# Kernel tuning notes

Hardware: AMD Instinct MI355X
Metric: run time of the kernel (lower is better)

## Reference

```python
import jax, jax.numpy as jnp
import numpy as np

BUCKET = 32   # bucket_size hard-coded in module
HEADS = 8
LN_EPS = 1e-5
SELF_ATTN_VALUE = -5e4  # TOKEN_SELF_ATTN_VALUE from reformer-pytorch


def _layer_norm(x, g, b):
    m = jnp.mean(x, axis=-1, keepdims=True)
    v = jnp.mean((x - m) ** 2, axis=-1, keepdims=True)
    return (x - m) / jnp.sqrt(v + LN_EPS) * g + b


def _lsh_attention(qk, v, rot):
    # qk, v: (B=b*h, T, Dh); rot: (Dh, n_buckets//2); n_hashes = 1
    B, T, D = qk.shape
    n_buckets = T // BUCKET
    # hash: random rotations, argmax over [r, -r]
    r = jnp.einsum('btf,fi->bti', qk, rot)                 # (B, T, n_buckets//2)
    r = jnp.concatenate([r, -r], axis=-1)                  # (B, T, n_buckets)
    buckets = jnp.argmax(r, axis=-1)                       # (B, T) int
    t = jnp.arange(T)
    key = buckets * T + t                                  # unique sort key
    sticker = jnp.argsort(key, axis=-1)                    # (B, T) permutation
    undo = jnp.argsort(sticker, axis=-1)
    sqk = jnp.take_along_axis(qk, sticker[..., None], axis=1)
    sv = jnp.take_along_axis(v, sticker[..., None], axis=1)
    # chunk into n_buckets chunks of size BUCKET
    bq_t = sticker.reshape(B, n_buckets, BUCKET)
    bq = sqk.reshape(B, n_buckets, BUCKET, D)
    bv = sv.reshape(B, n_buckets, BUCKET, D)
    nrm = jnp.sqrt(jnp.sum(bq * bq, axis=-1, keepdims=True))
    bk = bq / jnp.maximum(nrm, 1e-12)                      # shared-QK: keys are unit-norm queries
    def look_one_back(xx):
        return jnp.concatenate([xx, jnp.roll(xx, 1, axis=1)], axis=2)
    bk = look_one_back(bk)
    bvv = look_one_back(bv)
    bkv_t = look_one_back(bq_t)
    dots = jnp.einsum('bcie,bcje->bcij', bq, bk) * (D ** -0.5)  # (B, C, 32, 64)
    self_mask = bq_t[:, :, :, None] == bkv_t[:, :, None, :]
    dots = jnp.where(self_mask, SELF_ATTN_VALUE, dots)
    attn = jax.nn.softmax(dots, axis=-1)
    bo = jnp.einsum('bcij,bcje->bcie', attn, bvv)
    so = bo.reshape(B, T, D)
    return jnp.take_along_axis(so, undo[..., None], axis=1)   # unsort (n_hashes=1 -> probs=1)


def _lsh_self_attention(h, w_qk, w_v, w_out, b_out, rot):
    b, t, d = h.shape
    dh = d // HEADS
    qk = (h @ w_qk).reshape(b, t, HEADS, dh).transpose(0, 2, 1, 3).reshape(b * HEADS, t, dh)
    vv = (h @ w_v).reshape(b, t, HEADS, dh).transpose(0, 2, 1, 3).reshape(b * HEADS, t, dh)
    o = _lsh_attention(qk, vv, rot)
    o = o.reshape(b, HEADS, t, dh).transpose(0, 2, 1, 3).reshape(b, t, d)
    return o @ w_out + b_out


def setup_inputs() -> dict:
    key = jax.random.key(0)
    ks = jax.random.split(key, 8)
    B, T, D, F = 8, 4096, 512, 2048
    dh, nb = D // HEADS, T // BUCKET
    s = 0.02
    return {
        'x': jax.random.normal(ks[0], (B, T, D), jnp.float32),
        'w_qk': jax.random.normal(ks[1], (D, D), jnp.float32) * s,
        'w_v': jax.random.normal(ks[2], (D, D), jnp.float32) * s,
        'w_out': jax.random.normal(ks[3], (D, D), jnp.float32) * s,
        'b_out': jnp.zeros((D,), jnp.float32),
        'ln1_g': jnp.ones((D,), jnp.float32),
        'ln1_b': jnp.zeros((D,), jnp.float32),
        'w_ff1': jax.random.normal(ks[4], (D, F), jnp.float32) * s,
        'b_ff1': jnp.zeros((F,), jnp.float32),
        'w_ff2': jax.random.normal(ks[5], (F, D), jnp.float32) * s,
        'b_ff2': jnp.zeros((D,), jnp.float32),
        'ln2_g': jnp.ones((D,), jnp.float32),
        'ln2_b': jnp.zeros((D,), jnp.float32),
        'rotations': jax.random.normal(ks[6], (dh, nb // 2), jnp.float32),
    }


def reference(x, w_qk, w_v, w_out, b_out, ln1_g, ln1_b, w_ff1, b_ff1,
              w_ff2, b_ff2, ln2_g, ln2_b, rotations):
    # y1 = x + Attn(LN1(x)); y2 = x + FFN(LN2(y1)); out = mean(y1, y2)
    h1 = _layer_norm(x, ln1_g, ln1_b)
    y1 = x + _lsh_self_attention(h1, w_qk, w_v, w_out, b_out, rotations)
    h2 = _layer_norm(y1, ln2_g, ln2_b)
    ffn = jax.nn.relu(h2 @ w_ff1 + b_ff1) @ w_ff2 + b_ff2
    y2 = x + ffn
    return 0.5 * (y1 + y2)
```

## Files before the change

kernel.cpp:

```cpp
#include <hip/hip_runtime.h>
#include <stdint.h>

typedef _Float16 f16;
typedef _Float16 f16x8 __attribute__((ext_vector_type(8)));
typedef float    f32x4 __attribute__((ext_vector_type(4)));
typedef unsigned long long u64;

__device__ __forceinline__ void gload16(const void* g, void* l) {
  __builtin_amdgcn_global_load_lds(
      (__attribute__((address_space(1))) void*)g,
      (__attribute__((address_space(3))) void*)l, 16, 0, 0);
}

#define MFMA_QUAD(q, af) \
  _Pragma("unroll") for (int m2 = 0; m2 < 2; ++m2) \
  _Pragma("unroll") for (int nt = 0; nt < 4; ++nt) \
  _Pragma("unroll") for (int kk = 0; kk < 2; ++kk) \
    acc[(q)*2 + m2][nt] = __builtin_amdgcn_mfma_f32_16x16x32_f16( \
        af[m2][kk], bf[nt][kk], acc[(q)*2 + m2][nt], 0, 0, 0);

#define RD_A(dst, abase, q2) \
  _Pragma("unroll") for (int m2 = 0; m2 < 2; ++m2) \
  _Pragma("unroll") for (int kk = 0; kk < 2; ++kk) { \
    const int lr = (q2)*32 + m2*16 + l15; \
    dst[m2][kk] = *(const f16x8*)&abase[lr*64 + (((kk*4 + l4) ^ (lr & 7)) << 3)]; }

#define RD_B(bbase) \
  _Pragma("unroll") for (int nt = 0; nt < 4; ++nt) \
  _Pragma("unroll") for (int kk = 0; kk < 2; ++kk) { \
    const int lr = brow + nt*16 + l15; \
    bf[nt][kk] = *(const f16x8*)&bbase[lr*64 + (((kk*4 + l4) ^ (lr & 7)) << 3)]; }

#define PH_PRE() \
  __builtin_amdgcn_s_barrier(); \
  asm volatile("s_waitcnt lgkmcnt(0)" ::: "memory"); \
  __builtin_amdgcn_sched_barrier(0); \
  __builtin_amdgcn_s_setprio(1);

#define PH_POST() \
  __builtin_amdgcn_s_setprio(0); \
  __builtin_amdgcn_s_barrier(); \
  __builtin_amdgcn_sched_barrier(0);

template<int EPI>
__global__ __launch_bounds__(512, 2)
void gemm256(const f16* __restrict__ A, int lda,
             const f16* __restrict__ Bt, int ldb,
             int K, int N,
             float* __restrict__ outf, f16* __restrict__ outh,
             f16* __restrict__ outh2,
             const float* __restrict__ bias,
             const f16* __restrict__ sxyh,
             const float* __restrict__ add1)
{
  __shared__ __align__(16) f16 lds[65536];
  const int tid = threadIdx.x, lane = tid & 63;
  const int wid = tid >> 6;
  const int wm = wid >> 2, wn = wid & 3;
  const int l15 = lane & 15, l4 = lane >> 4;

  const int gx = gridDim.x;
  int lid = blockIdx.y * gx + blockIdx.x;
  const int cpx = (gx * gridDim.y) >> 3;
  lid = (lid & 7) * cpx + (lid >> 3);
  const long bm0 = (long)(lid / gx) * 256;
  const long bn0 = (long)(lid % gx) * 256;

  const int rs = tid >> 3, cs = tid & 7;
  const int cg = cs ^ (rs & 7);
  const int nkt = K >> 6;
  const int nmask = nkt - 1;

  auto stageA = [&](int d, int half, int kt) {
    f16* dst = &lds[(d * 4 + half) * 8192];
    const long kb = (long)kt * 64 + cg * 8;
    const f16* src = A + (bm0 + half * 128) * lda + kb;
#pragma unroll
    for (int rr = 0; rr < 2; ++rr) {
      const int row = rs + rr * 64;
      gload16(src + (long)row * lda, dst + row * 64 + cs * 8);
    }
  };
  auto stageB = [&](int d, int half, int kt) {
    f16* dst = &lds[(d * 4 + 2 + half) * 8192];
    const long kb = (long)kt * 64 + cg * 8;
    const f16* src = Bt + (bn0 + half * 128) * ldb + kb;
#pragma unroll
    for (int rr = 0; rr < 2; ++rr) {
      const int row = rs + rr * 64;
      gload16(src + (long)row * ldb, dst + row * 64 + cs * 8);
    }
  };

  const f16* aBase0 = &lds[(0 + wm) * 8192];
  const f16* aBase1 = &lds[(4 + wm) * 8192];
  const f16* bBase0 = &lds[(2 + (wn >> 1)) * 8192];
  const f16* bBase1 = &lds[(6 + (wn >> 1)) * 8192];
  const int brow = (wn & 1) * 64;

  f32x4 acc[8][4];
#pragma unroll
  for (int i = 0; i < 8; ++i)
#pragma unroll
    for (int j = 0; j < 4; ++j) acc[i][j] = f32x4{0.f, 0.f, 0.f, 0.f};
  f16x8 bf[4][2], afA[2][2], afB[2][2];

  stageB(0, 0, 0); stageB(0, 1, 0); stageA(0, 0, 0); stageA(0, 1, 0);
  asm volatile("s_waitcnt vmcnt(4)" ::: "memory");
  stageB(1, 0, 1); stageB(1, 1, 1); stageA(1, 0, 1);
  asm volatile("s_waitcnt vmcnt(6)" ::: "memory");
  __builtin_amdgcn_s_barrier();
  __builtin_amdgcn_sched_barrier(0);

  for (int j = 0; j < nkt; j += 2) {
    const int t2 = (j + 2) & nmask, t3 = (j + 3) & nmask;
    RD_B(bBase0); RD_A(afA, aBase0, 0);
    stageA(1, 1, j + 1);
    asm volatile("s_waitcnt lgkmcnt(8)" ::: "memory");
    PH_PRE(); MFMA_QUAD(0, afA); PH_POST();
    RD_A(afB, aBase0, 1); RD_A(afA, aBase0, 2);
    stageB(0, 0, t2);
    PH_PRE(); MFMA_QUAD(1, afB); PH_POST();
    RD_A(afB, aBase0, 3);
    stageB(0, 1, t2);
    PH_PRE(); MFMA_QUAD(2, afA); PH_POST();
    stageA(0, 0, t2);
    asm volatile("s_waitcnt vmcnt(6)" ::: "memory");
    PH_PRE(); MFMA_QUAD(3, afB); PH_POST();
    RD_B(bBase1); RD_A(afA, aBase1, 0);
    stageA(0, 1, t2);
    asm volatile("s_waitcnt lgkmcnt(8)" ::: "memory");
    PH_PRE(); MFMA_QUAD(0, afA); PH_POST();
    RD_A(afB, aBase1, 1); RD_A(afA, aBase1, 2);
    stageB(1, 0, t3);
    PH_PRE(); MFMA_QUAD(1, afB); PH_POST();
    RD_A(afB, aBase1, 3);
    stageB(1, 1, t3);
    PH_PRE(); MFMA_QUAD(2, afA); PH_POST();
    stageA(1, 0, t3);
    asm volatile("s_waitcnt vmcnt(6)" ::: "memory");
    PH_PRE(); MFMA_QUAD(3, afB); PH_POST();
  }
  asm volatile("s_waitcnt vmcnt(0)" ::: "memory");

  if constexpr (EPI == 17) {
    const int hcol = (int)(bn0 >> 6) + wn;
    const int is_v = hcol >> 3, h = hcol & 7;
    f16* base = is_v ? outh2 : outh;
#pragma unroll
    for (int mt = 0; mt < 8; ++mt)
#pragma unroll
      for (int r = 0; r < 4; ++r) {
        const long grow = bm0 + wm * 128 + mt * 16 + l4 * 4 + r;
        const int bb = (int)(grow >> 12), tt = (int)(grow & 4095);
        f16* dst = base + (((long)bb * 8 + h) * 4096 + tt) * 64;
#pragma unroll
        for (int nt = 0; nt < 4; ++nt)
          dst[nt * 16 + l15] = (f16)acc[mt][nt][0 * 4 + 0];
      }
  }
#pragma unroll
  for (int mt = 0; mt < 8; ++mt)
#pragma unroll
    for (int nt = 0; nt < 4; ++nt)
#pragma unroll
      for (int r = 0; r < 4; ++r) {
        const long grow = bm0 + wm * 128 + mt * 16 + l4 * 4 + r;
        const long gcol = bn0 + wn * 64 + nt * 16 + l15;
        const float c = acc[mt][nt][r];
        if constexpr (EPI == 12) {
          const long idx = grow * (long)N + gcol;
          outf[idx] = c + bias[gcol] + add1[idx];
        } else if constexpr (EPI == 13) {
          const long idx = grow * (long)N + gcol;
          outh[idx] = (f16)fmaxf(c + bias[gcol], 0.f);
        } else if constexpr (EPI == 40) {
          const long idx = grow * (long)N + gcol;
          outf[idx] = (float)sxyh[idx] + 0.5f * c;
        } else if constexpr (EPI == 41) {
          const long idx = grow * (long)N + gcol;
          outf[idx] += 0.5f * (c + bias[gcol]);
        } else if constexpr (EPI == 17) {
          const int bb = (int)(grow >> 12), tt = (int)(grow & 4095);
          const int hcol = (int)(bn0 >> 6) + wn;
          const int is_v = hcol >> 3, h = hcol & 7;
          f16* base = is_v ? outh2 : outh;
          base[(((long)bb * 8 + h) * 4096 + tt) * 64 + nt * 16 + l15] = (f16)c;
        }
      }
}

__global__ __launch_bounds__(256)
void ln_kernel(const float* __restrict__ in, const float* __restrict__ gam,
               const float* __restrict__ bet, f16* __restrict__ out,
               int ldo, int split, const float* __restrict__ xin,
               f16* __restrict__ sxy)
{
  const long row = (long)blockIdx.x * 4 + (threadIdx.x >> 6);
  const int lane = threadIdx.x & 63;
  const float4* p = (const float4*)(in + row * 512);
  const float4 a = p[lane * 2], b = p[lane * 2 + 1];
  float xv[8] = {a.x, a.y, a.z, a.w, b.x, b.y, b.z, b.w};
  float s = 0.f;
#pragma unroll
  for (int i = 0; i < 8; ++i) s += xv[i];
#pragma unroll
  for (int m = 32; m; m >>= 1) s += __shfl_xor(s, m);
  const float mean = s * (1.f / 512.f);
  float vs = 0.f;
#pragma unroll
  for (int i = 0; i < 8; ++i) { const float d = xv[i] - mean; vs += d * d; }
#pragma unroll
  for (int m = 32; m; m >>= 1) vs += __shfl_xor(vs, m);
  const float rstd = 1.f / sqrtf(vs * (1.f / 512.f) + 1e-5f);
  const float4* gp = (const float4*)gam;
  const float4* bp = (const float4*)bet;
  const float4 g0 = gp[lane * 2], g1 = gp[lane * 2 + 1];
  const float4 b0 = bp[lane * 2], b1 = bp[lane * 2 + 1];
  const float gg[8] = {g0.x, g0.y, g0.z, g0.w, g1.x, g1.y, g1.z, g1.w};
  const float bb[8] = {b0.x, b0.y, b0.z, b0.w, b1.x, b1.y, b1.z, b1.w};
  f16x8 vh, vl;
#pragma unroll
  for (int i = 0; i < 8; ++i) {
    const float y = (xv[i] - mean) * rstd * gg[i] + bb[i];
    const f16 hi = (f16)y;
    vh[i] = hi;
    vl[i] = (f16)((y - (float)hi) * 64.f);
  }
  f16* o = out + row * ldo + lane * 8;
  *(f16x8*)o = vh;
  if (split) *(f16x8*)(o + 512) = vl;
  if (sxy) {
    const float4* xp = (const float4*)(xin + row * 512);
    const float4 x0 = xp[lane * 2], x1 = xp[lane * 2 + 1];
    const float xx[8] = {x0.x, x0.y, x0.z, x0.w, x1.x, x1.y, x1.z, x1.w};
    f16x8 vsx;
#pragma unroll
    for (int i = 0; i < 8; ++i) vsx[i] = (f16)(0.5f * (xv[i] + xx[i]));
    *(f16x8*)(sxy + row * 512 + lane * 8) = vsx;
  }
}

__global__ __launch_bounds__(256)
void transpose_f16(const float* __restrict__ src, f16* __restrict__ dst, int K, int N)
{
  __shared__ float tile[32][33];
  const int tx = threadIdx.x & 31, ty = threadIdx.x >> 5;
  const long k0 = (long)blockIdx.y * 32, n0 = (long)blockIdx.x * 32;
#pragma unroll
  for (int i = 0; i < 4; ++i)
    tile[ty + i * 8][tx] = src[(k0 + ty + i * 8) * N + n0 + tx];
  __syncthreads();
#pragma unroll
  for (int i = 0; i < 4; ++i)
    dst[(n0 + ty + i * 8) * K + k0 + tx] = (f16)tile[tx][ty + i * 8];
}

__global__ __launch_bounds__(256)
void whash_f32(const float* __restrict__ wqk, const float* __restrict__ rot,
               float* __restrict__ WrT, f16* __restrict__ rotTh)
{
  if (blockIdx.x == 0 && blockIdx.y == 0) {
    for (int idx = threadIdx.x; idx < 4096; idx += 256) {
      const int d = idx >> 6, i = idx & 63;
      rotTh[i * 64 + d] = (f16)rot[idx];
    }
  }
  const int kk = blockIdx.x;
  const int n  = blockIdx.y * 256 + threadIdx.x;
  const int h = n >> 6, i = n & 63;
  float s = 0.f;
  for (int d = 0; d < 64; ++d)
    s += wqk[kk * 512 + h * 64 + d] * rot[d * 64 + i];
  WrT[(long)n * 512 + kk] = s;
}

__global__ __launch_bounds__(256)
void rhash4_kernel(const f16* __restrict__ gqk, const f16* __restrict__ rotTh,
                   int* __restrict__ buckets)
{
  const int tid = threadIdx.x, lane = tid & 63, w = tid >> 6;
  const int bh = blockIdx.x >> 5, tb = blockIdx.x & 31;
  const int t0 = tb * 128;
  const int l15 = lane & 15, l4 = lane >> 4;

  f16x8 br[2][4];
#pragma unroll
  for (int kk = 0; kk < 2; ++kk)
#pragma unroll
    for (int nt = 0; nt < 4; ++nt)
      br[kk][nt] = *(const f16x8*)&rotTh[(nt * 16 + l15) * 64 + kk * 32 + l4 * 8];

  const f16* gqb = gqk + ((long)bh * 4096 + t0) * 64;
  f16x8 aq[2][2];
#pragma unroll
  for (int kk = 0; kk < 2; ++kk)
#pragma unroll
    for (int mt = 0; mt < 2; ++mt)
      aq[kk][mt] = *(const f16x8*)&gqb[(long)(w * 32 + mt * 16 + l15) * 64 + kk * 32 + l4 * 8];

  f32x4 acc[2][4];
#pragma unroll
  for (int i = 0; i < 2; ++i)
#pragma unroll
    for (int j = 0; j < 4; ++j) acc[i][j] = f32x4{0.f, 0.f, 0.f, 0.f};
#pragma unroll
  for (int kk = 0; kk < 2; ++kk)
#pragma unroll
    for (int mt = 0; mt < 2; ++mt)
#pragma unroll
      for (int nt = 0; nt < 4; ++nt)
        acc[mt][nt] = __builtin_amdgcn_mfma_f32_16x16x32_f16(aq[kk][mt], br[kk][nt], acc[mt][nt], 0, 0, 0);

#pragma unroll
  for (int mt = 0; mt < 2; ++mt)
#pragma unroll
    for (int r = 0; r < 4; ++r) {
      const float v0 = acc[mt][0][r], v1 = acc[mt][1][r];
      const float v2 = acc[mt][2][r], v3 = acc[mt][3][r];
      unsigned int k0 = (__float_as_uint(fabsf(v0)) & ~63u) | (unsigned int)(63 - l15);
      unsigned int k1 = (__float_as_uint(fabsf(v1)) & ~63u) | (unsigned int)(47 - l15);
      unsigned int k2 = (__float_as_uint(fabsf(v2)) & ~63u) | (unsigned int)(31 - l15);
      unsigned int k3 = (__float_as_uint(fabsf(v3)) & ~63u) | (unsigned int)(15 - l15);
      float ss = v0 * v0 + v1 * v1 + v2 * v2 + v3 * v3;
#pragma unroll
      for (int m = 1; m < 16; m <<= 1) ss += __shfl_xor(ss, m);

      unsigned int mk = max(max(k0, k1), max(k2, k3));
#pragma unroll
      for (int m = 1; m < 16; m <<= 1) mk = max(mk, (unsigned int)__shfl_xor((int)mk, m));
      const unsigned int key1 = mk;
      const int col1 = 63 - (int)(key1 & 63u);
      const float m1f = __uint_as_float(key1 & ~63u);
      const int nt1 = col1 >> 4;
      const float vsel = (nt1 == 0) ? v0 : (nt1 == 1) ? v1 : (nt1 == 2) ? v2 : v3;
      const bool owner = (col1 & 15) == l15;
      const u64 bal = __ballot(owner && (vsel < 0.f));
      const int neg = (int)((bal >> (l4 * 16 + (col1 & 15))) & 1ull);
      const int bucket = col1 + (neg << 6);
      if (owner) {
        if (nt1 == 0) k0 = 0; else if (nt1 == 1) k1 = 0;
        else if (nt1 == 2) k2 = 0; else k3 = 0;
      }
      mk = max(max(k0, k1), max(k2, k3));
#pragma unroll
      for (int m = 1; m < 16; m <<= 1) mk = max(mk, (unsigned int)__shfl_xor((int)mk, m));
      const int col2 = 63 - (int)(mk & 63u);
      const float m2f = __uint_as_float(mk & ~63u);
      {
        const int nt2 = col2 >> 4;
        if ((col2 & 15) == l15) {
          if (nt2 == 0) k0 = 0; else if (nt2 == 1) k1 = 0;
          else if (nt2 == 2) k2 = 0; else k3 = 0;
        }
      }
      mk = max(max(k0, k1), max(k2, k3));
#pragma unroll
      for (int m = 1; m < 16; m <<= 1) mk = max(mk, (unsigned int)__shfl_xor((int)mk, m));
      const int col3 = 63 - (int)(mk & 63u);

      if (l15 == 0) {
        const int row = w * 32 + mt * 16 + l4 * 4 + r;
        const int bht = bh * 4096 + t0 + row;
        const float margin = m1f - m2f;
        const float rms = sqrtf(ss * (1.f / 64.f));
        const int flag = (margin < 0.015f * rms) ? 1 : 0;
        buckets[bht] = bucket | (col2 << 8) | (col3 << 16) | (flag << 24);
      }
    }
}

__global__ __launch_bounds__(256)
void fixup2_kernel(const f16* __restrict__ hsplit, const float* __restrict__ WrT,
                   int* __restrict__ buckets)
{
  const int wid = (blockIdx.x * 256 + threadIdx.x) >> 6;
  const int lane = threadIdx.x & 63;
  for (int batch = 0; batch < 4; ++batch) {
    const int base = wid * 256 + batch * 64;
    const int packed = buckets[base + lane];
    u64 bal = __ballot((packed >> 24) & 1);
    while (bal) {
      const int i = (int)__ffsll((long long)bal) - 1;
      bal &= bal - 1;
      const int row = base + i;
      const int pk = __shfl(packed, i);
      const int h = (row >> 12) & 7;
      const long hrow = (long)(row >> 15) * 4096 + (row & 4095);
      const f16* hp = hsplit + hrow * 1024 + lane * 8;
      const f16x8 hi = *(const f16x8*)hp;
      const f16x8 lo = *(const f16x8*)(hp + 512);
      float h1[8];
#pragma unroll
      for (int k = 0; k < 8; ++k) h1[k] = (float)hi[k] + (float)lo[k] * 0.015625f;
      const int cols[3] = { pk & 63, (pk >> 8) & 63, (pk >> 16) & 63 };
      float best = -1e30f; int bi = 999;
#pragma unroll
      for (int c = 0; c < 3; ++c) {
        const int cc = cols[c];
        const float* wp = WrT + ((long)(h * 64 + cc)) * 512 + lane * 8;
        const float4 w0 = *(const float4*)wp;
        const float4 w1 = *(const float4*)(wp + 4);
        float s = h1[0] * w0.x + h1[1] * w0.y + h1[2] * w0.z + h1[3] * w0.w
                + h1[4] * w1.x + h1[5] * w1.y + h1[6] * w1.z + h1[7] * w1.w;
#pragma unroll
        for (int m = 32; m; m >>= 1) s += __shfl_xor(s, m);
        if (s > best || (s == best && cc < bi)) { best = s; bi = cc; }
        const float ns = -s; const int ni = 64 + cc;
        if (ns > best || (ns == best && ni < bi)) { best = ns; bi = ni; }
      }
      if (lane == 0) buckets[row] = bi;
    }
  }
}

__global__ __launch_bounds__(256)
void sort_kernel(const int* __restrict__ buckets, int* __restrict__ sticker)
{
  __shared__ int bkt[4096];
  __shared__ unsigned int cnts[64][128];
  __shared__ unsigned char rnk[4096];
  __shared__ int tot[128];
  __shared__ int base[128];
  const int bh = blockIdx.x;
  const int tid = threadIdx.x;
  const int lane = tid & 63, wv = tid >> 6;

  for (int i = tid; i < 4096; i += 256) bkt[i] = buckets[(long)bh * 4096 + i] & 127;
  for (int i = tid; i < 64 * 128; i += 256) ((unsigned int*)cnts)[i] = 0u;
  __syncthreads();

  for (int it = 0; it < 16; ++it) {
    const int c = wv * 16 + it;
    const int t = c * 64 + lane;
    const int b = bkt[t];
    unsigned long long m = ~0ull;
#pragma unroll
    for (int k = 0; k < 7; ++k) {
      const bool bit = (b >> k) & 1;
      const unsigned long long bal = __ballot(bit);
      m &= bit ? bal : ~bal;
    }
    const int rk = (int)__popcll(m & ((1ull << lane) - 1ull));
    rnk[t] = (unsigned char)rk;
    if (rk == 0) cnts[c][b] = (unsigned int)__popcll(m);
  }
  __syncthreads();

  if (tid < 128) {
    unsigned int run = 0;
    for (int c = 0; c < 64; ++c) {
      const unsigned int x = cnts[c][tid];
      cnts[c][tid] = run;
      run += x;
    }
    tot[tid] = (int)run;
  }
  __syncthreads();
  if (tid == 0) {
    int run = 0;
    for (int b = 0; b < 128; ++b) { base[b] = run; run += tot[b]; }
  }
  __syncthreads();

  for (int it = 0; it < 16; ++it) {
    const int c = wv * 16 + it;
    const int t = c * 64 + lane;
    const int b = bkt[t];
    const int pos = base[b] + (int)cnts[c][b] + (int)rnk[t];
    sticker[(long)bh * 4096 + pos] = t;
  }
}

__global__ __launch_bounds__(256)
void attn2_kernel(const f16* __restrict__ gqk, const f16* __restrict__ gv,
                  const int* __restrict__ sticker, f16* __restrict__ o)
{
  __shared__ __align__(16) f16 sqk[160 * 64];
  __shared__ __align__(16) f16 sVT[64 * 168];
  __shared__ __align__(16) f16 sP[4][32 * 72];
  __shared__ float rnorm[160];
  __shared__ int st[160];

  const int tid = threadIdx.x, lane = tid & 63, w = tid >> 6;
  const int cg = blockIdx.x, bh = blockIdx.y;
  const int b = bh >> 3, h = bh & 7;
  const int p0 = cg * 128 - 32;
  const int l15 = lane & 15, l4 = lane >> 4;

  if (tid < 160) st[tid] = sticker[(long)bh * 4096 + ((p0 + tid) & 4095)] & 4095;
  __syncthreads();

  const f16* gqb = gqk + (long)bh * 4096 * 64;
#pragma unroll
  for (int it = 0; it < 5; ++it) {
    const int idx = it * 256 + tid;
    const int row = idx >> 3, ch = idx & 7;
    const int gsrc = ch ^ (row & 7);
    gload16(gqb + (long)st[row] * 64 + gsrc * 8, &sqk[idx * 8]);
  }

  const f16* gvb = gv + (long)bh * 4096 * 64;
  f16x8 va[5];
#pragma unroll
  for (int i = 0; i < 5; ++i) {
    const int row = w * 40 + i * 8 + (lane >> 3);
    va[i] = *(const f16x8*)&gvb[(long)st[row] * 64 + (lane & 7) * 8];
  }
#pragma unroll
  for (int i = 0; i < 5; ++i) {
    const int row = w * 40 + i * 8 + (lane >> 3);
    const int d0 = (lane & 7) * 8;
#pragma unroll
    for (int e = 0; e < 8; ++e) sVT[(d0 + e) * 168 + row] = va[i][e];
  }
  __syncthreads();

  if (tid < 160) {
    float s = 0.f;
#pragma unroll
    for (int g = 0; g < 8; ++g) {
      const f16x8 v = *(const f16x8*)&sqk[tid * 64 + ((g ^ (tid & 7)) << 3)];
#pragma unroll
      for (int e = 0; e < 8; ++e) { const float f = (float)v[e]; s += f * f; }
    }
    rnorm[tid] = 1.f / fmaxf(sqrtf(s), 1e-12f);
  }
  __syncthreads();

  f32x4 acc[2][4];
#pragma unroll
  for (int i = 0; i < 2; ++i)
#pragma unroll
    for (int j = 0; j < 4; ++j) acc[i][j] = f32x4{0.f, 0.f, 0.f, 0.f};

#pragma unroll
  for (int kk = 0; kk < 2; ++kk) {
    f16x8 aq[2], bk[4];
#pragma unroll
    for (int mt = 0; mt < 2; ++mt) {
      const int row = 32 + w * 32 + mt * 16 + l15;
      const int g = kk * 4 + l4;
      aq[mt] = *(const f16x8*)&sqk[row * 64 + ((g ^ (row & 7)) << 3)];
    }
#pragma unroll
    for (int nt = 0; nt < 4; ++nt) {
      const int row = w * 32 + nt * 16 + l15;
      const int g = kk * 4 + l4;
      bk[nt] = *(const f16x8*)&sqk[row * 64 + ((g ^ (row & 7)) << 3)];
    }
#pragma unroll
    for (int mt = 0; mt < 2; ++mt)
#pragma unroll
      for (int nt = 0; nt < 4; ++nt)
        acc[mt][nt] = __builtin_amdgcn_mfma_f32_16x16x32_f16(aq[mt], bk[nt], acc[mt][nt], 0, 0, 0);
  }

  float rn[4];
#pragma unroll
  for (int nt = 0; nt < 4; ++nt) rn[nt] = rnorm[w * 32 + nt * 16 + l15];

  float pinv[2][4];
#pragma unroll
  for (int mt = 0; mt < 2; ++mt)
#pragma unroll
    for (int r = 0; r < 4; ++r) {
      const int row_i = mt * 16 + l4 * 4 + r;
      float mx = -1e30f;
#pragma unroll
      for (int nt = 0; nt < 4; ++nt) {
        float v = acc[mt][nt][r] * 0.125f * rn[nt];
        if (nt * 16 + l15 == row_i + 32) v = -5e4f;
        acc[mt][nt][r] = v;
        mx = fmaxf(mx, v);
      }
#pragma unroll
      for (int m = 8; m; m >>= 1) mx = fmaxf(mx, __shfl_xor(mx, m));
      float ssum = 0.f;
#pragma unroll
      for (int nt = 0; nt < 4; ++nt) {
        const float pe = expf(acc[mt][nt][r] - mx);
        ssum += pe;
        sP[w][row_i * 72 + nt * 16 + l15] = (f16)pe;
      }
#pragma unroll
      for (int m = 8; m; m >>= 1) ssum += __shfl_xor(ssum, m);
      pinv[mt][r] = 1.f / ssum;
    }
  __syncthreads();

  f32x4 pacc[2][4];
#pragma unroll
  for (int i = 0; i < 2; ++i)
#pragma unroll
    for (int j = 0; j < 4; ++j) pacc[i][j] = f32x4{0.f, 0.f, 0.f, 0.f};

#pragma unroll
  for (int kk = 0; kk < 2; ++kk) {
    f16x8 ap[2], bv[4];
#pragma unroll
    for (int mt = 0; mt < 2; ++mt)
      ap[mt] = *(const f16x8*)&sP[w][(mt * 16 + l15) * 72 + kk * 32 + l4 * 8];
#pragma unroll
    for (int nt = 0; nt < 4; ++nt)
      bv[nt] = *(const f16x8*)&sVT[(nt * 16 + l15) * 168 + w * 32 + kk * 32 + l4 * 8];
#pragma unroll
    for (int mt = 0; mt < 2; ++mt)
#pragma unroll
      for (int nt = 0; nt < 4; ++nt)
        pacc[mt][nt] = __builtin_amdgcn_mfma_f32_16x16x32_f16(ap[mt], bv[nt], pacc[mt][nt], 0, 0, 0);
  }

  const long ob = (long)b * 4096 * 512 + h * 64;
#pragma unroll
  for (int mt = 0; mt < 2; ++mt)
#pragma unroll
    for (int r = 0; r < 4; ++r) {
      const int row_i = mt * 16 + l4 * 4 + r;
      const long t = st[32 + w * 32 + row_i];
      const float sc = pinv[mt][r];
#pragma unroll
      for (int nt = 0; nt < 4; ++nt)
        o[ob + t * 512 + nt * 16 + l15] = (f16)(pacc[mt][nt][r] * sc);
    }
}

extern "C" void kernel_launch(void* const* d_in, const int* in_sizes, int n_in,
                              void* d_out, int out_size, void* d_ws, size_t ws_size,
                              hipStream_t stream)
{
  const float* x     = (const float*)d_in[0];
  const float* w_qk  = (const float*)d_in[1];
  const float* w_v   = (const float*)d_in[2];
  const float* w_out = (const float*)d_in[3];
  const float* b_out = (const float*)d_in[4];
  const float* ln1g  = (const float*)d_in[5];
  const float* ln1b  = (const float*)d_in[6];
  const float* w_ff1 = (const float*)d_in[7];
  const float* b_ff1 = (const float*)d_in[8];
  const float* w_ff2 = (const float*)d_in[9];
  const float* b_ff2 = (const float*)d_in[10];
  const float* ln2g  = (const float*)d_in[11];
  const float* ln2b  = (const float*)d_in[12];
  const float* rot   = (const float*)d_in[13];
  float* out = (float*)d_out;

  char* ws = (char*)d_ws;
  f16* hsplit = (f16*)ws;
  f16* o_buf  = (f16*)ws;
  f16* sxy    = (f16*)ws;
  f16* h2     = (f16*)(ws + 33554432);
  f16* gqk    = (f16*)(ws + 67108864);
  f16* gv     = (f16*)(ws + 100663296);
  f16* abuf   = (f16*)(ws + 67108864);
  char* W0 = ws + 134217728;
  f16* wqkvT = (f16*)W0;
  f16* woutT = (f16*)(W0 + 1048576);
  f16* wff1T = (f16*)(W0 + 1572864);
  f16* wff2T = (f16*)(W0 + 3670016);
  float* WrT = (float*)(W0 + 5767168);
  int* buckets = (int*)(W0 + 6815744);
  int* sticker = (int*)(W0 + 7864320);
  f16* rotTh   = (f16*)(W0 + 8912896);

  const dim3 b256(256);
  const dim3 b512(512);
  transpose_f16<<<dim3(16, 16), b256, 0, stream>>>(w_qk,  wqkvT,             512, 512);
  transpose_f16<<<dim3(16, 16), b256, 0, stream>>>(w_v,   wqkvT + 512 * 512, 512, 512);
  transpose_f16<<<dim3(16, 16), b256, 0, stream>>>(w_out, woutT,             512, 512);
  transpose_f16<<<dim3(64, 16), b256, 0, stream>>>(w_ff1, wff1T,             512, 2048);
  transpose_f16<<<dim3(16, 64), b256, 0, stream>>>(w_ff2, wff2T,             2048, 512);
  whash_f32<<<dim3(512, 2), b256, 0, stream>>>(w_qk, rot, WrT, rotTh);
  ln_kernel<<<dim3(8192), b256, 0, stream>>>(x, ln1g, ln1b, hsplit, 1024, 1, nullptr, nullptr);
  gemm256<17><<<dim3(4, 128), b512, 0, stream>>>(hsplit, 1024, wqkvT, 512, 512, 1024,
      nullptr, gqk, gv, nullptr, nullptr, nullptr);
  rhash4_kernel<<<dim3(2048), b256, 0, stream>>>(gqk, rotTh, buckets);
  fixup2_kernel<<<dim3(256), b256, 0, stream>>>(hsplit, WrT, buckets);
  sort_kernel<<<dim3(64), b256, 0, stream>>>(buckets, sticker);
  attn2_kernel<<<dim3(32, 64), b256, 0, stream>>>(gqk, gv, sticker, o_buf);
  gemm256<12><<<dim3(2, 128), b512, 0, stream>>>(o_buf, 512, woutT, 512, 512, 512,
      out, nullptr, nullptr, b_out, nullptr, x);
  ln_kernel<<<dim3(8192), b256, 0, stream>>>(out, ln2g, ln2b, h2, 512, 0, x, sxy);
  for (int f = 0; f < 2; ++f) {
    gemm256<13><<<dim3(4, 128), b512, 0, stream>>>(h2, 512, wff1T + (long)f * 1024 * 512, 512,
        512, 1024, nullptr, abuf, nullptr, b_ff1 + f * 1024, nullptr, nullptr);
    if (f == 0)
      gemm256<40><<<dim3(2, 128), b512, 0, stream>>>(abuf, 1024, wff2T + 1024 * 0, 2048,
          1024, 512, out, nullptr, nullptr, b_ff2, sxy, nullptr);
    else
      gemm256<41><<<dim3(2, 128), b512, 0, stream>>>(abuf, 1024, wff2T + 1024, 2048,
          1024, 512, out, nullptr, nullptr, b_ff2, sxy, nullptr);
  }
}
```

Measured before the change: 491.3 us.

## Split FFN by rows instead of hidden dim; add dedicated 128-tile FFN2 GEMM

The feed-forward block was previously split along the hidden dimension (two 1024-wide halves), with the second FFN2 pass doing a read-modify-write on the output. It is now split into two row chunks, each computing the full 2048-wide FFN1 and then a new 128x128-tile GEMM kernel for FFN2 with K=2048 that writes the final output in one pass. The new FFN2 kernel uses a simple single-buffered LDS loop instead of the pipelined 256-tile kernel, which may reduce overlap but gives more blocks for the N=512 output. Dead epilogue variants and an unused pointer argument are removed, and a K-tile index is masked.

```diff
diff --git a/kernel.cpp b/kernel.cpp
--- a/kernel.cpp
+++ b/kernel.cpp
@@ -50,7 +50,6 @@
              float* __restrict__ outf, f16* __restrict__ outh,
              f16* __restrict__ outh2,
              const float* __restrict__ bias,
-             const f16* __restrict__ sxyh,
              const float* __restrict__ add1)
 {
   __shared__ __align__(16) f16 lds[65536];
@@ -115,7 +114,7 @@
   for (int j = 0; j < nkt; j += 2) {
     const int t2 = (j + 2) & nmask, t3 = (j + 3) & nmask;
     RD_B(bBase0); RD_A(afA, aBase0, 0);
-    stageA(1, 1, j + 1);
+    stageA(1, 1, (j + 1) & nmask);
     asm volatile("s_waitcnt lgkmcnt(8)" ::: "memory");
     PH_PRE(); MFMA_QUAD(0, afA); PH_POST();
     RD_A(afB, aBase0, 1); RD_A(afA, aBase0, 2);
@@ -143,22 +142,6 @@
   }
   asm volatile("s_waitcnt vmcnt(0)" ::: "memory");
 
-  if constexpr (EPI == 17) {
-    const int hcol = (int)(bn0 >> 6) + wn;
-    const int is_v = hcol >> 3, h = hcol & 7;
-    f16* base = is_v ? outh2 : outh;
-#pragma unroll
-    for (int mt = 0; mt < 8; ++mt)
-#pragma unroll
-      for (int r = 0; r < 4; ++r) {
-        const long grow = bm0 + wm * 128 + mt * 16 + l4 * 4 + r;
-        const int bb = (int)(grow >> 12), tt = (int)(grow & 4095);
-        f16* dst = base + (((long)bb * 8 + h) * 4096 + tt) * 64;
-#pragma unroll
-        for (int nt = 0; nt < 4; ++nt)
-          dst[nt * 16 + l15] = (f16)acc[mt][nt][0 * 4 + 0];
-      }
-  }
 #pragma unroll
   for (int mt = 0; mt < 8; ++mt)
 #pragma unroll
@@ -174,12 +157,6 @@
         } else if constexpr (EPI == 13) {
           const long idx = grow * (long)N + gcol;
           outh[idx] = (f16)fmaxf(c + bias[gcol], 0.f);
-        } else if constexpr (EPI == 40) {
-          const long idx = grow * (long)N + gcol;
-          outf[idx] = (float)sxyh[idx] + 0.5f * c;
-        } else if constexpr (EPI == 41) {
-          const long idx = grow * (long)N + gcol;
-          outf[idx] += 0.5f * (c + bias[gcol]);
         } else if constexpr (EPI == 17) {
           const int bb = (int)(grow >> 12), tt = (int)(grow & 4095);
           const int hcol = (int)(bn0 >> 6) + wn;
@@ -187,6 +164,88 @@
           f16* base = is_v ? outh2 : outh;
           base[(((long)bb * 8 + h) * 4096 + tt) * 64 + nt * 16 + l15] = (f16)c;
         }
+      }
+}
+
+__global__ __launch_bounds__(512)
+void gemm8_ffn2(const f16* __restrict__ A,
+                const f16* __restrict__ Bt,
+                const f16* __restrict__ sxyh,
+                const float* __restrict__ bias,
+                float* __restrict__ outf)
+{
+  __shared__ __align__(16) f16 sA[128 * 64];
+  __shared__ __align__(16) f16 sB[128 * 64];
+  const int tid  = threadIdx.x;
+  const int lane = tid & 63;
+  const int wv   = tid >> 6;
+  const int wm   = wv >> 2, wn = wv & 3;
+  const int l15  = lane & 15, l4 = lane >> 4;
+
+  const int gx = gridDim.x;
+  int lid = blockIdx.y * gx + blockIdx.x;
+  const int cpx = (gx * gridDim.y) >> 3;
+  lid = (lid & 7) * cpx + (lid >> 3);
+  const long bm0 = (long)(lid / gx) * 128;
+  const long bn0 = (long)(lid % gx) * 128;
+
+  f32x4 acc[4][2];
+#pragma unroll
+  for (int i = 0; i < 4; ++i)
+#pragma unroll
+    for (int j = 0; j < 2; ++j) acc[i][j] = f32x4{0.f, 0.f, 0.f, 0.f};
+
+  const int rs = tid >> 3;
+  const int cs = tid & 7;
+  const int cg = cs ^ (rs & 7);
+
+  for (int kt = 0; kt < 32; ++kt) {
+    __syncthreads();
+    const long ka = (long)kt * 64 + cg * 8;
+#pragma unroll
+    for (int rd = 0; rd < 2; ++rd) {
+      const int row = rs + rd * 64;
+      gload16(A + (bm0 + row) * 2048 + ka, &sA[row * 64 + cs * 8]);
+    }
+#pragma unroll
+    for (int rd = 0; rd < 2; ++rd) {
+      const int row = rs + rd * 64;
+      gload16(Bt + (bn0 + row) * 2048 + ka, &sB[row * 64 + cs * 8]);
+    }
+    __syncthreads();
+#pragma unroll
+    for (int kk = 0; kk < 2; ++kk) {
+      f16x8 af[4], bfr[2];
+#pragma unroll
+      for (int mt = 0; mt < 4; ++mt) {
+        const int row = wm * 64 + mt * 16 + l15;
+        const int c = kk * 4 + l4;
+        af[mt] = *(const f16x8*)&sA[row * 64 + ((c ^ (row & 7)) << 3)];
+      }
+#pragma unroll
+      for (int nt = 0; nt < 2; ++nt) {
+        const int row = wn * 32 + nt * 16 + l15;
+        const int c = kk * 4 + l4;
+        bfr[nt] = *(const f16x8*)&sB[row * 64 + ((c ^ (row & 7)) << 3)];
+      }
+#pragma unroll
+      for (int mt = 0; mt < 4; ++mt)
+#pragma unroll
+        for (int nt = 0; nt < 2; ++nt)
+          acc[mt][nt] = __builtin_amdgcn_mfma_f32_16x16x32_f16(af[mt], bfr[nt], acc[mt][nt], 0, 0, 0);
+    }
+  }
+
+#pragma unroll
+  for (int mt = 0; mt < 4; ++mt)
+#pragma unroll
+    for (int nt = 0; nt < 2; ++nt)
+#pragma unroll
+      for (int r = 0; r < 4; ++r) {
+        const long grow = bm0 + wm * 64 + mt * 16 + l4 * 4 + r;
+        const long gcol = bn0 + wn * 32 + nt * 16 + l15;
+        const long idx  = grow * 512 + gcol;
+        outf[idx] = (float)sxyh[idx] + 0.5f * (acc[mt][nt][r] + bias[gcol]);
       }
 }
 
@@ -673,22 +732,19 @@
   whash_f32<<<dim3(512, 2), b256, 0, stream>>>(w_qk, rot, WrT, rotTh);
   ln_kernel<<<dim3(8192), b256, 0, stream>>>(x, ln1g, ln1b, hsplit, 1024, 1, nullptr, nullptr);
   gemm256<17><<<dim3(4, 128), b512, 0, stream>>>(hsplit, 1024, wqkvT, 512, 512, 1024,
-      nullptr, gqk, gv, nullptr, nullptr, nullptr);
+      nullptr, gqk, gv, nullptr, nullptr);
   rhash4_kernel<<<dim3(2048), b256, 0, stream>>>(gqk, rotTh, buckets);
   fixup2_kernel<<<dim3(256), b256, 0, stream>>>(hsplit, WrT, buckets);
   sort_kernel<<<dim3(64), b256, 0, stream>>>(buckets, sticker);
   attn2_kernel<<<dim3(32, 64), b256, 0, stream>>>(gqk, gv, sticker, o_buf);
   gemm256<12><<<dim3(2, 128), b512, 0, stream>>>(o_buf, 512, woutT, 512, 512, 512,
-      out, nullptr, nullptr, b_out, nullptr, x);
+      out, nullptr, nullptr, b_out, x);
   ln_kernel<<<dim3(8192), b256, 0, stream>>>(out, ln2g, ln2b, h2, 512, 0, x, sxy);
-  for (int f = 0; f < 2; ++f) {
-    gemm256<13><<<dim3(4, 128), b512, 0, stream>>>(h2, 512, wff1T + (long)f * 1024 * 512, 512,
-        512, 1024, nullptr, abuf, nullptr, b_ff1 + f * 1024, nullptr, nullptr);
-    if (f == 0)
-      gemm256<40><<<dim3(2, 128), b512, 0, stream>>>(abuf, 1024, wff2T + 1024 * 0, 2048,
-          1024, 512, out, nullptr, nullptr, b_ff2, sxy, nullptr);
-    else
-      gemm256<41><<<dim3(2, 128), b512, 0, stream>>>(abuf, 1024, wff2T + 1024, 2048,
-          1024, 512, out, nullptr, nullptr, b_ff2, sxy, nullptr);
-  }
-}
+  for (int c = 0; c < 2; ++c) {
+    const long roff = (long)c * 16384;
+    gemm256<13><<<dim3(8, 64), b512, 0, stream>>>(h2 + roff * 512, 512, wff1T, 512,
+        512, 2048, nullptr, abuf, nullptr, b_ff1, nullptr);
+    gemm8_ffn2<<<dim3(4, 128), b512, 0, stream>>>(abuf, wff2T, sxy + roff * 512,
+        b_ff2, out + roff * 512);
+  }
+}
```

After: 468.4 us. 1.05x faster.
